# Kernel optimization log

Hardware: AMD Instinct MI355X
Metric: run time of the kernel (lower is better)

## Reference

```python
import jax, jax.numpy as jnp
import numpy as np
from jax import lax

# OpenCV GaussianBlur(ksize=5, sigma=0) uses the fixed tabulated kernel [1,4,6,4,1]/16
_G1 = np.array([1.0, 4.0, 6.0, 4.0, 1.0], np.float32) / 16.0
GAUSS_K = jnp.asarray(np.outer(_G1, _G1))  # (5,5)
_D2 = np.array([1.0, 0.0, -2.0, 0.0, 1.0], np.float32)
_S = np.array([1.0, 4.0, 6.0, 4.0, 1.0], np.float32)
LAP_K = jnp.asarray(np.outer(_S, _D2) + np.outer(_D2, _S))  # (5,5)


def _conv2d_reflect101(img, k):
    # img: (N, h, w); k: (5,5). OpenCV default border = BORDER_REFLECT_101 == jnp 'reflect'
    p = jnp.pad(img, ((0, 0), (2, 2), (2, 2)), mode='reflect')
    out = lax.conv_general_dilated(p[:, None], k[None, None], (1, 1), 'VALID')
    return out[:, 0]


def reference(x):
    b, s, c, h, w = x.shape
    # grayscale per image: mean over channels
    g = x.mean(axis=2).reshape(b * s, h, w)
    blurred = _conv2d_reflect101(g, GAUSS_K)
    lap = _conv2d_reflect101(blurred, LAP_K).reshape(b, s, h, w)
    # sharpest frame per pixel (laplacian replicated over channels in original,
    # so argmax is channel-independent)
    idx = jnp.argmax(lap, axis=1)  # (b, h, w)
    idx = jnp.broadcast_to(idx[:, None, None, :, :], (b, 1, c, h, w))
    merged = jnp.take_along_axis(x, idx, axis=1)[:, 0]  # (b, c, h, w)
    return merged


def setup_inputs() -> dict:
    key = jax.random.key(0)
    x = jax.random.normal(key, (4, 8, 3, 1024, 1024), dtype=jnp.float32)
    return {"x": x}
```

## Files before the change

kernel.cpp:

```cpp
#include <hip/hip_runtime.h>

#define BB 4
#define SS 8
#define CC 3
#define HH 1024
#define WW 1024
#define TH 32
#define TW 64
#define GSH (TH + 8)
#define GSW (TW + 8)
#define HBH (TH + 8)
#define HBW (TW + 4)
#define BLH (TH + 4)
#define BLW (TW + 4)

__device__ __forceinline__ int refl(int i, int n) {
    i = (i < 0) ? -i : i;
    i = (i >= n) ? (2 * n - 2 - i) : i;
    return i;
}

__global__ __launch_bounds__(256, 2)
void lap_focus_mixed(const float* __restrict__ x, float* __restrict__ out) {
    const int tile = blockIdx.x;
    const int b  = tile >> 9;
    const int t  = tile & 511;
    const int tr = t >> 4;
    const int tc = t & 15;
    const int r0 = tr * TH;
    const int c0 = tc * TW;

    __shared__ float  gs[GSH][GSW];
    __shared__ double hb[HBH][HBW];
    __shared__ float  bl[BLH][BLW];

    const int tid = threadIdx.x;
    const int tx = tid & 63;
    const int ty = tid >> 6;

    float best[8];
    int   bidx[8];
#pragma unroll
    for (int m = 0; m < 8; ++m) { best[m] = -3.0e38f; bidx[m] = 0; }

    const double GA[5] = {0.0625, 0.25, 0.375, 0.25, 0.0625};
    const double LW[5][5] = {
        { 2.,  4.,   4.,  4.,  2.},
        { 4.,  0.,  -8.,  0.,  4.},
        { 4., -8., -24., -8.,  4.},
        { 4.,  0.,  -8.,  0.,  4.},
        { 2.,  4.,   4.,  4.,  2.},
    };

    int ccol[5];
#pragma unroll
    for (int dj = 0; dj < 5; ++dj)
        ccol[dj] = refl(c0 + tx + dj - 2, WW) - c0 + 2;

    const size_t HW = (size_t)HH * WW;

    for (int s = 0; s < SS; ++s) {
        const float* xs = x + (size_t)((b * SS + s) * CC) * HW;

        for (int e = tid; e < GSH * GSW; e += 256) {
            int r = e / GSW;
            int c = e - r * GSW;
            int gi = refl(r0 + r - 4, HH);
            int gj = refl(c0 + c - 4, WW);
            size_t off = (size_t)gi * WW + gj;
            float v = (xs[off] + xs[HW + off]) + xs[2 * HW + off];
            gs[r][c] = v / 3.0f;
        }
        __syncthreads();

        for (int e = tid; e < HBH * HBW; e += 256) {
            int r = e / HBW;
            int c = e - r * HBW;
            double acc = 0.0;
#pragma unroll
            for (int j = 0; j < 5; ++j)
                acc += (double)gs[r][c + j] * GA[j];
            hb[r][c] = acc;
        }
        __syncthreads();

        for (int e = tid; e < BLH * BLW; e += 256) {
            int r = e / BLW;
            int c = e - r * BLW;
            double acc = 0.0;
#pragma unroll
            for (int i = 0; i < 5; ++i)
                acc += hb[r + i][c] * GA[i];
            bl[r][c] = (float)acc;
        }
        __syncthreads();

#pragma unroll
        for (int m = 0; m < 8; ++m) {
            int i = ty + 4 * m;
            double acc = 0.0;
#pragma unroll
            for (int di = 0; di < 5; ++di) {
                int rr = refl(r0 + i + di - 2, HH) - r0 + 2;
#pragma unroll
                for (int dj = 0; dj < 5; ++dj) {
                    if (LW[di][dj] != 0.0)
                        acc += (double)bl[rr][ccol[dj]] * LW[di][dj];
                }
            }
            float lap = (float)acc;
            if (lap > best[m]) { best[m] = lap; bidx[m] = s; }
        }
        __syncthreads();
    }

#pragma unroll
    for (int m = 0; m < 8; ++m) {
        int i = ty + 4 * m;
        int gi = r0 + i;
        int gj = c0 + tx;
        size_t off = (size_t)gi * WW + gj;
        const float* xs = x + (size_t)((b * SS + bidx[m]) * CC) * HW + off;
        float* op = out + (size_t)(b * CC) * HW + off;
        op[0]      = xs[0];
        op[HW]     = xs[HW];
        op[2 * HW] = xs[2 * HW];
    }
}

extern "C" void kernel_launch(void* const* d_in, const int* in_sizes, int n_in,
                              void* d_out, int out_size, void* d_ws, size_t ws_size,
                              hipStream_t stream) {
    (void)in_sizes; (void)n_in; (void)d_ws; (void)ws_size; (void)out_size;
    const float* x = (const float*)d_in[0];
    float* out = (float*)d_out;
    dim3 grid(BB * (HH / TH) * (WW / TW));
    dim3 block(256);
    hipLaunchKernelGGL(lap_focus_mixed, grid, block, 0, stream, x, out);
}
```

Baseline: 711.6 us.

## Fuse separable blur passes in registers and overlap next-frame gray load

Merges the horizontal and vertical Gaussian passes into one register-resident sliding window per column strip. This removes the double-precision shared-memory intermediate buffer and one barrier per frame. The grayscale load for the next frame now runs before the Laplacian stage of the current frame, so global loads overlap with compute, and the occupancy hint is raised to 6 blocks. Each strip recomputes 4 halo rows, and only 204 of 256 threads do blur work.

```diff
diff --git a/kernel.cpp b/kernel.cpp
--- a/kernel.cpp
+++ b/kernel.cpp
@@ -9,10 +9,12 @@
 #define TW 64
 #define GSH (TH + 8)
 #define GSW (TW + 8)
-#define HBH (TH + 8)
-#define HBW (TW + 4)
 #define BLH (TH + 4)
 #define BLW (TW + 4)
+#define NSTRIP 3
+#define RBS 12
+#define HBS (RBS + 4)
+#define NSLOT (NSTRIP * BLW)
 
 __device__ __forceinline__ int refl(int i, int n) {
     i = (i < 0) ? -i : i;
@@ -20,8 +22,8 @@
     return i;
 }
 
-__global__ __launch_bounds__(256, 2)
-void lap_focus_mixed(const float* __restrict__ x, float* __restrict__ out) {
+__global__ __launch_bounds__(256, 6)
+void lap_focus_fused(const float* __restrict__ x, float* __restrict__ out) {
     const int tile = blockIdx.x;
     const int b  = tile >> 9;
     const int t  = tile & 511;
@@ -30,9 +32,8 @@
     const int r0 = tr * TH;
     const int c0 = tc * TW;
 
-    __shared__ float  gs[GSH][GSW];
-    __shared__ double hb[HBH][HBW];
-    __shared__ float  bl[BLH][BLW];
+    __shared__ float gs[GSH][GSW];
+    __shared__ float bl[BLH][BLW];
 
     const int tid = threadIdx.x;
     const int tx = tid & 63;
@@ -57,11 +58,15 @@
     for (int dj = 0; dj < 5; ++dj)
         ccol[dj] = refl(c0 + tx + dj - 2, WW) - c0 + 2;
 
+    const bool slot_active = (tid < NSLOT);
+    const int strip = tid / BLW;
+    const int scol  = tid - strip * BLW;
+    const int hr0   = strip * RBS;
+
     const size_t HW = (size_t)HH * WW;
 
-    for (int s = 0; s < SS; ++s) {
+    auto load_gray = [&](int s) {
         const float* xs = x + (size_t)((b * SS + s) * CC) * HW;
-
         for (int e = tid; e < GSH * GSW; e += 256) {
             int r = e / GSW;
             int c = e - r * GSW;
@@ -71,29 +76,34 @@
             float v = (xs[off] + xs[HW + off]) + xs[2 * HW + off];
             gs[r][c] = v / 3.0f;
         }
-        __syncthreads();
+    };
 
-        for (int e = tid; e < HBH * HBW; e += 256) {
-            int r = e / HBW;
-            int c = e - r * HBW;
-            double acc = 0.0;
+    load_gray(0);
+    __syncthreads();
+
+    for (int s = 0; s < SS; ++s) {
+        if (slot_active) {
+            double w[5];
 #pragma unroll
-            for (int j = 0; j < 5; ++j)
-                acc += (double)gs[r][c + j] * GA[j];
-            hb[r][c] = acc;
+            for (int k = 0; k < HBS; ++k) {
+                double acc = 0.0;
+#pragma unroll
+                for (int j = 0; j < 5; ++j)
+                    acc += (double)gs[hr0 + k][scol + j] * GA[j];
+                w[k % 5] = acc;
+                if (k >= 4) {
+                    const int rb = k - 4;
+                    double a2 = 0.0;
+#pragma unroll
+                    for (int i = 0; i < 5; ++i)
+                        a2 += w[(rb + i) % 5] * GA[i];
+                    bl[hr0 + rb][scol] = (float)a2;
+                }
+            }
         }
         __syncthreads();
 
-        for (int e = tid; e < BLH * BLW; e += 256) {
-            int r = e / BLW;
-            int c = e - r * BLW;
-            double acc = 0.0;
-#pragma unroll
-            for (int i = 0; i < 5; ++i)
-                acc += hb[r + i][c] * GA[i];
-            bl[r][c] = (float)acc;
-        }
-        __syncthreads();
+        if (s + 1 < SS) load_gray(s + 1);
 
 #pragma unroll
         for (int m = 0; m < 8; ++m) {
@@ -136,5 +146,5 @@
     float* out = (float*)d_out;
     dim3 grid(BB * (HH / TH) * (WW / TW));
     dim3 block(256);
-    hipLaunchKernelGGL(lap_focus_mixed, grid, block, 0, stream, x, out);
+    hipLaunchKernelGGL(lap_focus_fused, grid, block, 0, stream, x, out);
 }
```

Result: slower. 788.4 us (+10.8%).
